# Optimization experiments

Measured on AMD Instinct MI355X. Metric: run time of the kernel, lower is better.

The kernel has to match this reference:

```python
import jax, jax.numpy as jnp
import numpy as np

NS, NV = 32, 8                      # scalar / vector multiplicities (32x0e + 8x1o)
N_NODES, N_EDGES = 16384, 131072
NEF, HID = 128, 128                 # edge feature dim, MLP hidden
WN = NS*NS + NV*NS + NS*NV + NV*NV  # 1600 tensor-product weights per edge
D = NS + 3*NV                       # 56 node feature dim
INV_SQRT3 = 1.0/np.sqrt(3.0)        # CG coeff for 1o x 1o -> 0e
PATH_NORM = 1.0/np.sqrt(NS + NV)    # fan-in normalization per output irrep
EPS = 1e-5


def setup_inputs() -> dict:
    key = jax.random.key(0)
    ks = jax.random.split(key, 10)
    node_attr = jax.random.normal(ks[0], (N_NODES, D), jnp.float32)
    edge_index = jax.random.randint(ks[1], (2, N_EDGES), 0, N_NODES, dtype=jnp.int64)
    edge_attr = jax.random.normal(ks[2], (N_EDGES, NEF), jnp.float32)
    edge_sh = jax.random.normal(ks[3], (N_EDGES, 4), jnp.float32)
    W1 = jax.random.normal(ks[4], (NEF, HID), jnp.float32) / np.sqrt(NEF)
    b1 = jnp.zeros((HID,), jnp.float32)
    W2 = jax.random.normal(ks[5], (HID, WN), jnp.float32) / np.sqrt(HID)
    b2 = jnp.zeros((WN,), jnp.float32)
    bn_gamma = jnp.ones((NS + NV,), jnp.float32)   # per-irrep scale (scalars then vectors)
    bn_beta = jnp.zeros((NS,), jnp.float32)        # bias only on scalar irreps
    return dict(node_attr=node_attr, edge_attr=edge_attr, edge_sh=edge_sh,
                W1=W1, b1=b1, W2=W2, b2=b2, bn_gamma=bn_gamma, bn_beta=bn_beta,
                edge_index=edge_index)


def reference(node_attr, edge_attr, edge_sh, W1, b1, W2, b2, bn_gamma, bn_beta, edge_index):
    edge_src, edge_dst = edge_index[0], edge_index[1]

    # per-edge tensor-product weights from edge MLP (dropout=0, eval mode)
    w = jax.nn.relu(edge_attr @ W1 + b1) @ W2 + b2            # [E, WN]
    o0 = NS*NS; o1 = o0 + NV*NS; o2 = o1 + NS*NV
    w_ss = w[:, :o0].reshape(-1, NS, NS)   # 0e x 0e -> 0e
    w_vs = w[:, o0:o1].reshape(-1, NV, NS) # 1o x 1o -> 0e
    w_sv = w[:, o1:o2].reshape(-1, NS, NV) # 0e x 1o -> 1o
    w_vv = w[:, o2:].reshape(-1, NV, NV)   # 1o x 0e -> 1o

    # gather node features onto edges
    x = node_attr[edge_dst]                # [E, D]
    xs = x[:, :NS]                         # [E, NS]
    xv = x[:, NS:].reshape(-1, NV, 3)      # [E, NV, 3]
    ss = edge_sh[:, 0]                     # [E]
    sv = edge_sh[:, 1:4]                   # [E, 3]

    # CG tensor product with per-edge fully-connected weights
    dot_vv = jnp.einsum('eim,em->ei', xv, sv) * INV_SQRT3
    out_s = (jnp.einsum('eij,ei->ej', w_ss, xs) * ss[:, None]
             + jnp.einsum('eij,ei->ej', w_vs, dot_vv)) * PATH_NORM          # [E, NS]
    out_v = (jnp.einsum('eij,ei->ej', w_sv, xs)[:, :, None] * sv[:, None, :]
             + jnp.einsum('eij,eim->ejm', w_vv, xv) * ss[:, None, None]) * PATH_NORM  # [E, NV, 3]
    tp = jnp.concatenate([out_s, out_v.reshape(-1, 3*NV)], axis=-1)         # [E, D]

    # scatter-mean to source nodes
    sums = jax.ops.segment_sum(tp, edge_src, num_segments=N_NODES)
    cnt = jax.ops.segment_sum(jnp.ones((tp.shape[0], 1), tp.dtype), edge_src,
                              num_segments=N_NODES)
    out = sums / jnp.maximum(cnt, 1.0)

    # residual (in/out irreps identical -> zero padding is a no-op)
    out = out + node_attr

    # equivariant batch norm (training-mode batch statistics)
    s = out[:, :NS]
    v = out[:, NS:].reshape(-1, NV, 3)
    s = (s - s.mean(0)) / jnp.sqrt(s.var(0) + EPS) * bn_gamma[:NS] + bn_beta
    vn2 = (v * v).sum(-1).mean(0)                               # [NV] mean squared norm
    v = v / jnp.sqrt(vn2 + EPS)[None, :, None] * bn_gamma[NS:][None, :, None]
    return jnp.concatenate([s, v.reshape(-1, 3*NV)], axis=-1)
```

## Files before the change

kernel.cpp:

```cpp
#include <hip/hip_runtime.h>

typedef short short8 __attribute__((ext_vector_type(8)));
typedef unsigned short us4 __attribute__((ext_vector_type(4)));
typedef float floatx4 __attribute__((ext_vector_type(4)));
typedef unsigned short u16;

#define NN 16384
#define NE 131072
#define NEF_ 128
#define DD 56
#define INV_SQRT3F 0.57735026918962576f
#define PATH_NORMF 0.15811388300841897f

__device__ __forceinline__ float bf2f(u16 u) {
    union { unsigned int i; float f; } v; v.i = ((unsigned int)u) << 16; return v.f;
}
__device__ __forceinline__ u16 f2bf(float f) {
    union { float f; unsigned int i; } v; v.f = f;
    unsigned int r = v.i + 0x7fffu + ((v.i >> 16) & 1u);
    return (u16)(r >> 16);
}

__global__ __launch_bounds__(256) void prep(const float* __restrict__ W1,
                                            const float* __restrict__ W2,
                                            u16* __restrict__ W1T,
                                            u16* __restrict__ W2T,
                                            const int* __restrict__ eidx,
                                            int* __restrict__ deg) {
    int b = blockIdx.x;
    if (b < 864) {
        int i = b * 256 + threadIdx.x;
        if (i < 16384) {
            int n = i >> 7, k = i & 127;
            W1T[i] = f2bf(W1[k * 128 + n]);
        } else {
            int j = i - 16384;
            int n = j >> 7, k = j & 127;
            W2T[j] = f2bf(W2[k * 1600 + n]);
        }
    } else {
        int e = (b - 864) * 256 + threadIdx.x;
        atomicAdd(&deg[eidx[e]], 1);
    }
}

__global__ __launch_bounds__(1024) void deg_scan(const int* __restrict__ deg,
                                                 int* __restrict__ row_start,
                                                 int* __restrict__ cursor) {
    __shared__ int part[1024];
    const int t = threadIdx.x;
    const int base = t * 16;
    int loc[16];
    int s = 0;
    #pragma unroll
    for (int i = 0; i < 16; i++) { loc[i] = s; s += deg[base + i]; }
    part[t] = s;
    __syncthreads();
    for (int off = 1; off < 1024; off <<= 1) {
        int v = (t >= off) ? part[t - off] : 0;
        __syncthreads();
        part[t] += v;
        __syncthreads();
    }
    int pre = (t == 0) ? 0 : part[t - 1];
    #pragma unroll
    for (int i = 0; i < 16; i++) {
        int v = pre + loc[i];
        row_start[base + i] = v;
        cursor[base + i] = v;
    }
    if (t == 1023) row_start[16384] = pre + s;
}

__global__ __launch_bounds__(256) void edge_scatter(const int* __restrict__ eidx,
                                                    int* __restrict__ cursor,
                                                    int* __restrict__ edge_order) {
    int e = blockIdx.x * 256 + threadIdx.x;
    int p = atomicAdd(&cursor[eidx[e]], 1);
    edge_order[p] = e;
}

__global__ __launch_bounds__(256, 2) void tpconv(
    const float* __restrict__ node_attr, const float* __restrict__ edge_attr,
    const float* __restrict__ edge_sh, const u16* __restrict__ W1T,
    const float* __restrict__ b1, const u16* __restrict__ W2T,
    const float* __restrict__ b2, const int* __restrict__ eidx,
    const int* __restrict__ edge_order,
    float* __restrict__ tp)
{
    __shared__ __align__(16) char smem[49920];
    u16*   sA  = (u16*)smem;
    u16*   sB  = (u16*)(smem + 17408);
    u16*   sF  = (u16*)(smem + 34816);
    float* b2s = (float*)(smem + 43520);
    float* Ssc  = (float*)smem;
    float* Svec = (float*)(smem + 16896);

    const int t = threadIdx.x;
    const int lane = t & 63;
    const int wv = t >> 6;
    const int m = lane & 15;
    const int q = lane >> 4;
    const int Rb = (wv >> 1) * 32;
    const int Cb = (wv & 1) * 32;
    const int p0 = blockIdx.x * 64;
    const int str = t >> 4;
    const int stc = (t & 15) * 8;

    short8 pre[4];
    #pragma unroll
    for (int ii = 0; ii < 4; ii++)
        pre[ii] = *(const short8*)&W2T[(size_t)(str + 16 * ii) * 128 + stc];

    for (int i = t; i < 1600; i += 256) b2s[i] = b2[i];

    #pragma unroll
    for (int ii = 0; ii < 8; ii++) {
        int cid = t + 256 * ii;
        int r = cid >> 5, s = cid & 31;
        int e = edge_order[p0 + r];
        const float* src = &edge_attr[(size_t)e * NEF_ + s * 4];
        us4 o;
        o.x = f2bf(src[0]); o.y = f2bf(src[1]); o.z = f2bf(src[2]); o.w = f2bf(src[3]);
        *(us4*)&sA[r * 136 + s * 4] = o;
    }
    if (t < 64) {
        int e = edge_order[p0 + t];
        int nd = eidx[NE + e];
        const float* na = node_attr + (size_t)nd * DD;
        const float* sh = edge_sh + (size_t)e * 4;
        float ss = sh[0], s0 = sh[1], s1 = sh[2], s2 = sh[3];
        #pragma unroll
        for (int i = 0; i < 32; i++) sF[i * 64 + t] = f2bf(na[i]);
        #pragma unroll
        for (int i = 0; i < 8; i++) {
            float d = (na[32+i*3]*s0 + na[33+i*3]*s1 + na[34+i*3]*s2) * INV_SQRT3F;
            sF[(32 + i) * 64 + t] = f2bf(d);
        }
        #pragma unroll
        for (int i = 0; i < 24; i++) sF[(40 + i) * 64 + t] = f2bf(na[32 + i]);
        sF[64 * 64 + t] = f2bf(ss);
        sF[65 * 64 + t] = f2bf(s0);
        sF[66 * 64 + t] = f2bf(s1);
        sF[67 * 64 + t] = f2bf(s2);
    }
    __syncthreads();

    floatx4 hacc[2][2][2];
    #pragma unroll
    for (int cc = 0; cc < 2; cc++) {
        #pragma unroll
        for (int ii = 0; ii < 4; ii++)
            *(short8*)&sB[(str + 16 * ii) * 136 + stc] =
                *(const short8*)&W1T[(size_t)(cc * 64 + str + 16 * ii) * 128 + stc];
        __syncthreads();
        #pragma unroll
        for (int rt = 0; rt < 2; rt++)
            #pragma unroll
            for (int ct = 0; ct < 2; ct++) {
                float bv = b1[cc * 64 + Cb + ct * 16 + m];
                hacc[cc][rt][ct] = (floatx4){bv, bv, bv, bv};
            }
        #pragma unroll
        for (int k0 = 0; k0 < 128; k0 += 32) {
            short8 a0 = *(const short8*)&sA[(Rb      + m) * 136 + k0 + q * 8];
            short8 a1 = *(const short8*)&sA[(Rb + 16 + m) * 136 + k0 + q * 8];
            short8 bA = *(const short8*)&sB[(Cb      + m) * 136 + k0 + q * 8];
            short8 bB = *(const short8*)&sB[(Cb + 16 + m) * 136 + k0 + q * 8];
            hacc[cc][0][0] = __builtin_amdgcn_mfma_f32_16x16x32_bf16(a0, bA, hacc[cc][0][0], 0, 0, 0);
            hacc[cc][0][1] = __builtin_amdgcn_mfma_f32_16x16x32_bf16(a0, bB, hacc[cc][0][1], 0, 0, 0);
            hacc[cc][1][0] = __builtin_amdgcn_mfma_f32_16x16x32_bf16(a1, bA, hacc[cc][1][0], 0, 0, 0);
            hacc[cc][1][1] = __builtin_amdgcn_mfma_f32_16x16x32_bf16(a1, bB, hacc[cc][1][1], 0, 0, 0);
        }
        __syncthreads();
    }
    #pragma unroll
    for (int cc = 0; cc < 2; cc++)
      #pragma unroll
      for (int rt = 0; rt < 2; rt++)
        #pragma unroll
        for (int ct = 0; ct < 2; ct++)
          #pragma unroll
          for (int r = 0; r < 4; r++) {
              int e   = Rb + rt * 16 + q * 4 + r;
              int col = cc * 64 + Cb + ct * 16 + m;
              float v = hacc[cc][rt][ct][r];
              sA[e * 136 + col] = f2bf(v > 0.f ? v : 0.f);
          }
    __syncthreads();

    short8 hc[4][4];
    #pragma unroll
    for (int et = 0; et < 4; et++)
        #pragma unroll
        for (int kk = 0; kk < 4; kk++)
            hc[et][kk] = *(const short8*)&sA[(et * 16 + m) * 136 + kk * 32 + q * 8];

    float ssc[4], svc[4][3];
    #pragma unroll
    for (int et = 0; et < 4; et++) {
        ssc[et] = bf2f(sF[64 * 64 + et * 16 + m]);
        svc[et][0] = bf2f(sF[65 * 64 + et * 16 + m]);
        svc[et][1] = bf2f(sF[66 * 64 + et * 16 + m]);
        svc[et][2] = bf2f(sF[67 * 64 + et * 16 + m]);
    }

    #pragma unroll
    for (int ii = 0; ii < 4; ii++)
        *(short8*)&sB[(str + 16 * ii) * 136 + stc] = pre[ii];
    #pragma unroll
    for (int ii = 0; ii < 4; ii++)
        pre[ii] = *(const short8*)&W2T[(size_t)(64 + str + 16 * ii) * 128 + stc];
    __syncthreads();

    float tps[4][4];
    float tpv[4][4][3];
    #pragma unroll
    for (int et = 0; et < 4; et++)
        #pragma unroll
        for (int r = 0; r < 4; r++) {
            tps[et][r] = 0.f;
            tpv[et][r][0] = 0.f; tpv[et][r][1] = 0.f; tpv[et][r][2] = 0.f;
        }

    for (int c = 0; c < 25; c++) {
        floatx4 bias = *(const floatx4*)&b2s[c * 64 + wv * 16 + q * 4];
        floatx4 acc[4];
        #pragma unroll
        for (int et = 0; et < 4; et++) acc[et] = bias;
        #pragma unroll
        for (int kk = 0; kk < 4; kk++) {
            short8 a = *(const short8*)&sB[(wv * 16 + m) * 136 + kk * 32 + q * 8];
            acc[0] = __builtin_amdgcn_mfma_f32_16x16x32_bf16(a, hc[0][kk], acc[0], 0, 0, 0);
            acc[1] = __builtin_amdgcn_mfma_f32_16x16x32_bf16(a, hc[1][kk], acc[1], 0, 0, 0);
            acc[2] = __builtin_amdgcn_mfma_f32_16x16x32_bf16(a, hc[2][kk], acc[2], 0, 0, 0);
            acc[3] = __builtin_amdgcn_mfma_f32_16x16x32_bf16(a, hc[3][kk], acc[3], 0, 0, 0);
        }

        if (c < 16) {
            const int i = 2 * c + (wv >> 1);
            #pragma unroll
            for (int et = 0; et < 4; et++) {
                float f = bf2f(sF[i * 64 + et * 16 + m]) * ssc[et];
                #pragma unroll
                for (int r = 0; r < 4; r++) tps[et][r] += acc[et][r] * f;
            }
        } else if (c < 20) {
            const int i = 2 * (c - 16) + (wv >> 1);
            #pragma unroll
            for (int et = 0; et < 4; et++) {
                float f = bf2f(sF[(32 + i) * 64 + et * 16 + m]);
                #pragma unroll
                for (int r = 0; r < 4; r++) tps[et][r] += acc[et][r] * f;
            }
        } else if (c < 24) {
            const int i = 8 * (c - 20) + wv * 2 + (q >> 1);
            #pragma unroll
            for (int et = 0; et < 4; et++) {
                float f = bf2f(sF[i * 64 + et * 16 + m]);
                #pragma unroll
                for (int r = 0; r < 4; r++) {
                    float t0 = acc[et][r] * f;
                    tpv[et][r][0] += t0 * svc[et][0];
                    tpv[et][r][1] += t0 * svc[et][1];
                    tpv[et][r][2] += t0 * svc[et][2];
                }
            }
        } else {
            const int i = wv * 2 + (q >> 1);
            #pragma unroll
            for (int et = 0; et < 4; et++) {
                float x0 = bf2f(sF[(40 + 3 * i + 0) * 64 + et * 16 + m]) * ssc[et];
                float x1 = bf2f(sF[(40 + 3 * i + 1) * 64 + et * 16 + m]) * ssc[et];
                float x2 = bf2f(sF[(40 + 3 * i + 2) * 64 + et * 16 + m]) * ssc[et];
                #pragma unroll
                for (int r = 0; r < 4; r++) {
                    tpv[et][r][0] += acc[et][r] * x0;
                    tpv[et][r][1] += acc[et][r] * x1;
                    tpv[et][r][2] += acc[et][r] * x2;
                }
            }
        }

        __syncthreads();
        if (c < 24) {
            #pragma unroll
            for (int ii = 0; ii < 4; ii++)
                *(short8*)&sB[(str + 16 * ii) * 136 + stc] = pre[ii];
            if (c < 23) {
                #pragma unroll
                for (int ii = 0; ii < 4; ii++)
                    pre[ii] = *(const short8*)&W2T[(size_t)((c + 2) * 64 + str + 16 * ii) * 128 + stc];
            }
        }
        __syncthreads();
    }

    #pragma unroll
    for (int et = 0; et < 4; et++)
        #pragma unroll
        for (int r = 0; r < 4; r++)
            Ssc[(wv >> 1) * 2112 + (et * 16 + m) * 33 + (wv & 1) * 16 + q * 4 + r] = tps[et][r];
    #pragma unroll
    for (int et = 0; et < 4; et++)
        #pragma unroll
        for (int r = 0; r < 4; r++)
            #pragma unroll
            for (int mm = 0; mm < 3; mm++) {
                float v = tpv[et][r][mm];
                v += __shfl_xor(v, 32, 64);
                if (q < 2)
                    Svec[wv * 1600 + (et * 16 + m) * 25 + ((q & 1) * 4 + r) * 3 + mm] = v;
            }
    __syncthreads();

    for (int idx = t; idx < 3584; idx += 256) {
        int e = idx / 56, d = idx - e * 56;
        float v;
        if (d < 32) {
            v = Ssc[e * 33 + d] + Ssc[2112 + e * 33 + d];
        } else {
            int dd = d - 32;
            v = Svec[e * 25 + dd] + Svec[1600 + e * 25 + dd]
              + Svec[3200 + e * 25 + dd] + Svec[4800 + e * 25 + dd];
        }
        tp[(size_t)(p0 + e) * DD + d] = v * PATH_NORMF;
    }
}

__global__ __launch_bounds__(256) void gather_finalize(
    const float* __restrict__ tp, const int* __restrict__ row_start,
    const float* __restrict__ node_attr,
    float* __restrict__ ybuf, float* __restrict__ partial)
{
    __shared__ float ps[4][72];
    const int wv = threadIdx.x >> 6, lane = threadIdx.x & 63;
    const int n = blockIdx.x * 4 + wv;
    const int beg = row_start[n], end = row_start[n + 1];
    if (lane < 56) {
        float acc = 0.f;
        for (int p = beg; p < end; p++)
            acc += tp[(size_t)p * DD + lane];
        float inv = 1.f / fmaxf((float)(end - beg), 1.f);
        float y = acc * inv + node_attr[(size_t)n * DD + lane];
        ybuf[(size_t)n * DD + lane] = y;
        if (lane < 32) {
            ps[wv][lane] = y;
            ps[wv][32 + lane] = y * y;
        } else {
            float vv = y * y;
            float v1 = __shfl_down(vv, 1, 64);
            float v2 = __shfl_down(vv, 2, 64);
            int l3 = lane - 32;
            if (l3 % 3 == 0) ps[wv][64 + l3 / 3] = vv + v1 + v2;
        }
    }
    __syncthreads();
    const int t = threadIdx.x;
    if (t < 72)
        partial[(size_t)blockIdx.x * 72 + t] = ps[0][t] + ps[1][t] + ps[2][t] + ps[3][t];
}

__global__ __launch_bounds__(256) void bn_reduce(const float* __restrict__ partial,
                                                 float* __restrict__ stats)
{
    __shared__ float red[256];
    const int d = blockIdx.x;
    const int t = threadIdx.x;
    float a = 0.f;
    for (int i = t; i < 4096; i += 256) a += partial[(size_t)i * 72 + d];
    red[t] = a;
    __syncthreads();
    for (int off = 128; off > 0; off >>= 1) {
        if (t < off) red[t] += red[t + off];
        __syncthreads();
    }
    if (t == 0) stats[d] = red[0] * (1.f / 16384.f);
}

__global__ __launch_bounds__(256) void bn_apply(
    const float* __restrict__ ybuf, const float* __restrict__ stats,
    const float* __restrict__ gamma, const float* __restrict__ beta,
    float* __restrict__ out)
{
    const int i = blockIdx.x * 256 + threadIdx.x;
    const int n = i / 56;
    const int d = i - n * 56;
    float y = ybuf[i];
    float o;
    if (d < 32) {
        float mn  = stats[d];
        float var = stats[32 + d] - mn * mn;
        o = (y - mn) * rsqrtf(var + 1e-5f) * gamma[d] + beta[d];
    } else {
        int jv = (d - 32) / 3;
        o = y * rsqrtf(stats[64 + jv] + 1e-5f) * gamma[32 + jv];
    }
    out[i] = o;
}

extern "C" void kernel_launch(void* const* d_in, const int* in_sizes, int n_in,
                              void* d_out, int out_size, void* d_ws, size_t ws_size,
                              hipStream_t stream)
{
    const float* node_attr = (const float*)d_in[0];
    const float* edge_attr = (const float*)d_in[1];
    const float* edge_sh   = (const float*)d_in[2];
    const float* W1        = (const float*)d_in[3];
    const float* b1        = (const float*)d_in[4];
    const float* W2        = (const float*)d_in[5];
    const float* b2        = (const float*)d_in[6];
    const float* gamma     = (const float*)d_in[7];
    const float* beta      = (const float*)d_in[8];
    const int*   eidx      = (const int*)d_in[9];

    char* ws = (char*)d_ws;
    u16*   W1T        = (u16*)(ws);
    u16*   W2T        = (u16*)(ws + 32768);
    int*   deg        = (int*)(ws + 442368);
    int*   row_start  = (int*)(ws + 507904);
    int*   cursor     = (int*)(ws + 573696);
    int*   edge_order = (int*)(ws + 639232);
    float* stats      = (float*)(ws + 1163520);
    float* partial    = (float*)(ws + 1164032);
    float* tp         = (float*)(ws + 2343680);
    float* ybuf       = (float*)(ws + 31703808);

    (void)hipMemsetAsync(deg, 0, 65536, stream);
    hipLaunchKernelGGL(prep,            dim3(1376), dim3(256),  0, stream,
                       W1, W2, W1T, W2T, eidx, deg);
    hipLaunchKernelGGL(deg_scan,        dim3(1),    dim3(1024), 0, stream, deg, row_start, cursor);
    hipLaunchKernelGGL(edge_scatter,    dim3(512),  dim3(256),  0, stream, eidx, cursor, edge_order);
    hipLaunchKernelGGL(tpconv,          dim3(2048), dim3(256),  0, stream,
                       node_attr, edge_attr, edge_sh, W1T, b1, W2T, b2, eidx, edge_order, tp);
    hipLaunchKernelGGL(gather_finalize, dim3(4096), dim3(256),  0, stream,
                       tp, row_start, node_attr, ybuf, partial);
    hipLaunchKernelGGL(bn_reduce,       dim3(72),   dim3(256),  0, stream, partial, stats);
    hipLaunchKernelGGL(bn_apply,        dim3(3584), dim3(256),  0, stream,
                       ybuf, stats, gamma, beta, (float*)d_out);
}
```

Before: 272.2 us.

## Split tpconv edge tile across 8 waves to cut per-thread registers

The tpconv block grows from 256 to 512 threads. The 64-edge tile is split into two 32-edge halves, each handled by four column-group waves, so every wave holds half as many accumulators, hidden fragments and tensor-product partial sums. The aim is lower register pressure and more resident waves per CU to hide latency, with launch bounds raised to 512,4. In exchange the W2 tile in LDS is read by twice as many waves, and the t<64 gather setup phase leaves more threads idle.

```diff
diff --git a/kernel.cpp b/kernel.cpp
--- a/kernel.cpp
+++ b/kernel.cpp
@@ -80,7 +80,7 @@
     edge_order[p] = e;
 }
 
-__global__ __launch_bounds__(256, 2) void tpconv(
+__global__ __launch_bounds__(512, 4) void tpconv(
     const float* __restrict__ node_attr, const float* __restrict__ edge_attr,
     const float* __restrict__ edge_sh, const u16* __restrict__ W1T,
     const float* __restrict__ b1, const u16* __restrict__ W2T,
@@ -101,22 +101,23 @@
     const int wv = t >> 6;
     const int m = lane & 15;
     const int q = lane >> 4;
-    const int Rb = (wv >> 1) * 32;
-    const int Cb = (wv & 1) * 32;
+    const int cg = wv & 3;
+    const int eh = wv >> 2;
+    const int eb = eh * 32;
     const int p0 = blockIdx.x * 64;
     const int str = t >> 4;
     const int stc = (t & 15) * 8;
 
-    short8 pre[4];
-    #pragma unroll
-    for (int ii = 0; ii < 4; ii++)
-        pre[ii] = *(const short8*)&W2T[(size_t)(str + 16 * ii) * 128 + stc];
-
-    for (int i = t; i < 1600; i += 256) b2s[i] = b2[i];
-
-    #pragma unroll
-    for (int ii = 0; ii < 8; ii++) {
-        int cid = t + 256 * ii;
+    short8 pre[2];
+    #pragma unroll
+    for (int ii = 0; ii < 2; ii++)
+        pre[ii] = *(const short8*)&W2T[(size_t)(str + 32 * ii) * 128 + stc];
+
+    for (int i = t; i < 1600; i += 512) b2s[i] = b2[i];
+
+    #pragma unroll
+    for (int ii = 0; ii < 4; ii++) {
+        int cid = t + 512 * ii;
         int r = cid >> 5, s = cid & 31;
         int e = edge_order[p0 + r];
         const float* src = &edge_attr[(size_t)e * NEF_ + s * 4];
@@ -146,31 +147,26 @@
     }
     __syncthreads();
 
-    floatx4 hacc[2][2][2];
+    floatx4 hacc[2][2];
     #pragma unroll
     for (int cc = 0; cc < 2; cc++) {
         #pragma unroll
-        for (int ii = 0; ii < 4; ii++)
-            *(short8*)&sB[(str + 16 * ii) * 136 + stc] =
-                *(const short8*)&W1T[(size_t)(cc * 64 + str + 16 * ii) * 128 + stc];
-        __syncthreads();
-        #pragma unroll
-        for (int rt = 0; rt < 2; rt++)
-            #pragma unroll
-            for (int ct = 0; ct < 2; ct++) {
-                float bv = b1[cc * 64 + Cb + ct * 16 + m];
-                hacc[cc][rt][ct] = (floatx4){bv, bv, bv, bv};
-            }
+        for (int ii = 0; ii < 2; ii++)
+            *(short8*)&sB[(str + 32 * ii) * 136 + stc] =
+                *(const short8*)&W1T[(size_t)(cc * 64 + str + 32 * ii) * 128 + stc];
+        __syncthreads();
+        {
+            float bv = b1[cc * 64 + cg * 16 + m];
+            hacc[cc][0] = (floatx4){bv, bv, bv, bv};
+            hacc[cc][1] = hacc[cc][0];
+        }
         #pragma unroll
         for (int k0 = 0; k0 < 128; k0 += 32) {
-            short8 a0 = *(const short8*)&sA[(Rb      + m) * 136 + k0 + q * 8];
-            short8 a1 = *(const short8*)&sA[(Rb + 16 + m) * 136 + k0 + q * 8];
-            short8 bA = *(const short8*)&sB[(Cb      + m) * 136 + k0 + q * 8];
-            short8 bB = *(const short8*)&sB[(Cb + 16 + m) * 136 + k0 + q * 8];
-            hacc[cc][0][0] = __builtin_amdgcn_mfma_f32_16x16x32_bf16(a0, bA, hacc[cc][0][0], 0, 0, 0);
-            hacc[cc][0][1] = __builtin_amdgcn_mfma_f32_16x16x32_bf16(a0, bB, hacc[cc][0][1], 0, 0, 0);
-            hacc[cc][1][0] = __builtin_amdgcn_mfma_f32_16x16x32_bf16(a1, bA, hacc[cc][1][0], 0, 0, 0);
-            hacc[cc][1][1] = __builtin_amdgcn_mfma_f32_16x16x32_bf16(a1, bB, hacc[cc][1][1], 0, 0, 0);
+            short8 a0 = *(const short8*)&sA[(eb      + m) * 136 + k0 + q * 8];
+            short8 a1 = *(const short8*)&sA[(eb + 16 + m) * 136 + k0 + q * 8];
+            short8 bA = *(const short8*)&sB[(cg * 16 + m) * 136 + k0 + q * 8];
+            hacc[cc][0] = __builtin_amdgcn_mfma_f32_16x16x32_bf16(a0, bA, hacc[cc][0], 0, 0, 0);
+            hacc[cc][1] = __builtin_amdgcn_mfma_f32_16x16x32_bf16(a1, bA, hacc[cc][1], 0, 0, 0);
         }
         __syncthreads();
     }
@@ -179,44 +175,42 @@
       #pragma unroll
       for (int rt = 0; rt < 2; rt++)
         #pragma unroll
-        for (int ct = 0; ct < 2; ct++)
-          #pragma unroll
-          for (int r = 0; r < 4; r++) {
-              int e   = Rb + rt * 16 + q * 4 + r;
-              int col = cc * 64 + Cb + ct * 16 + m;
-              float v = hacc[cc][rt][ct][r];
-              sA[e * 136 + col] = f2bf(v > 0.f ? v : 0.f);
-          }
-    __syncthreads();
-
-    short8 hc[4][4];
-    #pragma unroll
-    for (int et = 0; et < 4; et++)
+        for (int r = 0; r < 4; r++) {
+            int e   = eb + rt * 16 + q * 4 + r;
+            int col = cc * 64 + cg * 16 + m;
+            float v = hacc[cc][rt][r];
+            sA[e * 136 + col] = f2bf(v > 0.f ? v : 0.f);
+        }
+    __syncthreads();
+
+    short8 hc[2][4];
+    #pragma unroll
+    for (int et = 0; et < 2; et++)
         #pragma unroll
         for (int kk = 0; kk < 4; kk++)
-            hc[et][kk] = *(const short8*)&sA[(et * 16 + m) * 136 + kk * 32 + q * 8];
-
-    float ssc[4], svc[4][3];
-    #pragma unroll
-    for (int et = 0; et < 4; et++) {
-        ssc[et] = bf2f(sF[64 * 64 + et * 16 + m]);
-        svc[et][0] = bf2f(sF[65 * 64 + et * 16 + m]);
-        svc[et][1] = bf2f(sF[66 * 64 + et * 16 + m]);
-        svc[et][2] = bf2f(sF[67 * 64 + et * 16 + m]);
-    }
-
-    #pragma unroll
-    for (int ii = 0; ii < 4; ii++)
-        *(short8*)&sB[(str + 16 * ii) * 136 + stc] = pre[ii];
-    #pragma unroll
-    for (int ii = 0; ii < 4; ii++)
-        pre[ii] = *(const short8*)&W2T[(size_t)(64 + str + 16 * ii) * 128 + stc];
-    __syncthreads();
-
-    float tps[4][4];
-    float tpv[4][4][3];
-    #pragma unroll
-    for (int et = 0; et < 4; et++)
+            hc[et][kk] = *(const short8*)&sA[(eb + et * 16 + m) * 136 + kk * 32 + q * 8];
+
+    float ssc[2], svc[2][3];
+    #pragma unroll
+    for (int et = 0; et < 2; et++) {
+        ssc[et] = bf2f(sF[64 * 64 + eb + et * 16 + m]);
+        svc[et][0] = bf2f(sF[65 * 64 + eb + et * 16 + m]);
+        svc[et][1] = bf2f(sF[66 * 64 + eb + et * 16 + m]);
+        svc[et][2] = bf2f(sF[67 * 64 + eb + et * 16 + m]);
+    }
+
+    #pragma unroll
+    for (int ii = 0; ii < 2; ii++)
+        *(short8*)&sB[(str + 32 * ii) * 136 + stc] = pre[ii];
+    #pragma unroll
+    for (int ii = 0; ii < 2; ii++)
+        pre[ii] = *(const short8*)&W2T[(size_t)(64 + str + 32 * ii) * 128 + stc];
+    __syncthreads();
+
+    float tps[2][4];
+    float tpv[2][4][3];
+    #pragma unroll
+    for (int et = 0; et < 2; et++)
         #pragma unroll
         for (int r = 0; r < 4; r++) {
             tps[et][r] = 0.f;
@@ -224,40 +218,37 @@
         }
 
     for (int c = 0; c < 25; c++) {
-        floatx4 bias = *(const floatx4*)&b2s[c * 64 + wv * 16 + q * 4];
-        floatx4 acc[4];
-        #pragma unroll
-        for (int et = 0; et < 4; et++) acc[et] = bias;
+        floatx4 bias = *(const floatx4*)&b2s[c * 64 + cg * 16 + q * 4];
+        floatx4 acc[2];
+        acc[0] = bias; acc[1] = bias;
         #pragma unroll
         for (int kk = 0; kk < 4; kk++) {
-            short8 a = *(const short8*)&sB[(wv * 16 + m) * 136 + kk * 32 + q * 8];
+            short8 a = *(const short8*)&sB[(cg * 16 + m) * 136 + kk * 32 + q * 8];
             acc[0] = __builtin_amdgcn_mfma_f32_16x16x32_bf16(a, hc[0][kk], acc[0], 0, 0, 0);
             acc[1] = __builtin_amdgcn_mfma_f32_16x16x32_bf16(a, hc[1][kk], acc[1], 0, 0, 0);
-            acc[2] = __builtin_amdgcn_mfma_f32_16x16x32_bf16(a, hc[2][kk], acc[2], 0, 0, 0);
-            acc[3] = __builtin_amdgcn_mfma_f32_16x16x32_bf16(a, hc[3][kk], acc[3], 0, 0, 0);
         }
 
         if (c < 16) {
-            const int i = 2 * c + (wv >> 1);
-            #pragma unroll
-            for (int et = 0; et < 4; et++) {
-                float f = bf2f(sF[i * 64 + et * 16 + m]) * ssc[et];
+            const int i = 2 * c + (cg >> 1);
+            #pragma unroll
+            for (int et = 0; et < 2; et++) {
+                float f = bf2f(sF[i * 64 + eb + et * 16 + m]) * ssc[et];
                 #pragma unroll
                 for (int r = 0; r < 4; r++) tps[et][r] += acc[et][r] * f;
             }
         } else if (c < 20) {
-            const int i = 2 * (c - 16) + (wv >> 1);
-            #pragma unroll
-            for (int et = 0; et < 4; et++) {
-                float f = bf2f(sF[(32 + i) * 64 + et * 16 + m]);
+            const int i = 2 * (c - 16) + (cg >> 1);
+            #pragma unroll
+            for (int et = 0; et < 2; et++) {
+                float f = bf2f(sF[(32 + i) * 64 + eb + et * 16 + m]);
                 #pragma unroll
                 for (int r = 0; r < 4; r++) tps[et][r] += acc[et][r] * f;
             }
         } else if (c < 24) {
-            const int i = 8 * (c - 20) + wv * 2 + (q >> 1);
-            #pragma unroll
-            for (int et = 0; et < 4; et++) {
-                float f = bf2f(sF[i * 64 + et * 16 + m]);
+            const int i = 8 * (c - 20) + cg * 2 + (q >> 1);
+            #pragma unroll
+            for (int et = 0; et < 2; et++) {
+                float f = bf2f(sF[i * 64 + eb + et * 16 + m]);
                 #pragma unroll
                 for (int r = 0; r < 4; r++) {
                     float t0 = acc[et][r] * f;
@@ -267,12 +258,12 @@
                 }
             }
         } else {
-            const int i = wv * 2 + (q >> 1);
-            #pragma unroll
-            for (int et = 0; et < 4; et++) {
-                float x0 = bf2f(sF[(40 + 3 * i + 0) * 64 + et * 16 + m]) * ssc[et];
-                float x1 = bf2f(sF[(40 + 3 * i + 1) * 64 + et * 16 + m]) * ssc[et];
-                float x2 = bf2f(sF[(40 + 3 * i + 2) * 64 + et * 16 + m]) * ssc[et];
+            const int i = cg * 2 + (q >> 1);
+            #pragma unroll
+            for (int et = 0; et < 2; et++) {
+                float x0 = bf2f(sF[(40 + 3 * i + 0) * 64 + eb + et * 16 + m]) * ssc[et];
+                float x1 = bf2f(sF[(40 + 3 * i + 1) * 64 + eb + et * 16 + m]) * ssc[et];
+                float x2 = bf2f(sF[(40 + 3 * i + 2) * 64 + eb + et * 16 + m]) * ssc[et];
                 #pragma unroll
                 for (int r = 0; r < 4; r++) {
                     tpv[et][r][0] += acc[et][r] * x0;
@@ -285,24 +276,24 @@
         __syncthreads();
         if (c < 24) {
             #pragma unroll
-            for (int ii = 0; ii < 4; ii++)
-                *(short8*)&sB[(str + 16 * ii) * 136 + stc] = pre[ii];
+            for (int ii = 0; ii < 2; ii++)
+                *(short8*)&sB[(str + 32 * ii) * 136 + stc] = pre[ii];
             if (c < 23) {
                 #pragma unroll
-                for (int ii = 0; ii < 4; ii++)
-                    pre[ii] = *(const short8*)&W2T[(size_t)((c + 2) * 64 + str + 16 * ii) * 128 + stc];
-            }
-        }
-        __syncthreads();
-    }
-
-    #pragma unroll
-    for (int et = 0; et < 4; et++)
+                for (int ii = 0; ii < 2; ii++)
+                    pre[ii] = *(const short8*)&W2T[(size_t)((c + 2) * 64 + str + 32 * ii) * 128 + stc];
+            }
+        }
+        __syncthreads();
+    }
+
+    #pragma unroll
+    for (int et = 0; et < 2; et++)
         #pragma unroll
         for (int r = 0; r < 4; r++)
-            Ssc[(wv >> 1) * 2112 + (et * 16 + m) * 33 + (wv & 1) * 16 + q * 4 + r] = tps[et][r];
-    #pragma unroll
-    for (int et = 0; et < 4; et++)
+            Ssc[(cg >> 1) * 2112 + (eb + et * 16 + m) * 33 + (cg & 1) * 16 + q * 4 + r] = tps[et][r];
+    #pragma unroll
+    for (int et = 0; et < 2; et++)
         #pragma unroll
         for (int r = 0; r < 4; r++)
             #pragma unroll
@@ -310,11 +301,11 @@
                 float v = tpv[et][r][mm];
                 v += __shfl_xor(v, 32, 64);
                 if (q < 2)
-                    Svec[wv * 1600 + (et * 16 + m) * 25 + ((q & 1) * 4 + r) * 3 + mm] = v;
-            }
-    __syncthreads();
-
-    for (int idx = t; idx < 3584; idx += 256) {
+                    Svec[cg * 1600 + (eb + et * 16 + m) * 25 + ((q & 1) * 4 + r) * 3 + mm] = v;
+            }
+    __syncthreads();
+
+    for (int idx = t; idx < 3584; idx += 512) {
         int e = idx / 56, d = idx - e * 56;
         float v;
         if (d < 32) {
@@ -431,7 +422,7 @@
                        W1, W2, W1T, W2T, eidx, deg);
     hipLaunchKernelGGL(deg_scan,        dim3(1),    dim3(1024), 0, stream, deg, row_start, cursor);
     hipLaunchKernelGGL(edge_scatter,    dim3(512),  dim3(256),  0, stream, eidx, cursor, edge_order);
-    hipLaunchKernelGGL(tpconv,          dim3(2048), dim3(256),  0, stream,
+    hipLaunchKernelGGL(tpconv,          dim3(2048), dim3(512),  0, stream,
                        node_attr, edge_attr, edge_sh, W1T, b1, W2T, b2, eidx, edge_order, tp);
     hipLaunchKernelGGL(gather_finalize, dim3(4096), dim3(256),  0, stream,
                        tp, row_start, node_attr, ybuf, partial);
```

Result: faster. 256.2 us (-5.9%).
